# Kernel optimization log

Measured on AMD Instinct MI355X. Metric: run time of the kernel, lower is better.

The kernel has to match this reference:

```python
import jax, jax.numpy as jnp
import numpy as np


def _pairwise_sq_dist(a, b):
    # a: (B,N,D), b: (B,M,D) -> (B,N,M) squared euclidean distances
    # matmul trick matching torch.cdist (clamped at 0 before implicit sqrt)
    a2 = jnp.sum(a * a, axis=-1)  # (B,N)
    b2 = jnp.sum(b * b, axis=-1)  # (B,M)
    ab = jnp.einsum('bnd,bmd->bnm', a, b)  # (B,N,M)
    d2 = a2[:, :, None] + b2[:, None, :] - 2.0 * ab
    return jnp.maximum(d2, 0.0)


def setup_inputs() -> dict:
    key = jax.random.key(0)
    k1, k2 = jax.random.split(key)
    B, N, M, D = 8, 8192, 8192, 3
    gts = jax.random.normal(k1, (B, N, D), dtype=jnp.float32)
    preds = jax.random.normal(k2, (B, M, D), dtype=jnp.float32)
    return {"gts": gts, "preds": preds}


def reference(gts, preds):
    d2 = _pairwise_sq_dist(gts, preds)           # (B,N,M)
    min_g2p = jnp.min(d2, axis=2)                # (B,N) nearest pred for each gt
    min_p2g = jnp.min(d2, axis=1)                # (B,M) nearest gt for each pred
    return jnp.mean(min_g2p) + jnp.mean(min_p2g)
```

## Files before the change

### kernel.cpp

```cpp
#include <hip/hip_runtime.h>
#include <math.h>

#define BB 8
#define NN 8192
#define MM 8192

#define ROWS_PER_BLOCK 256
#define COLS_PER_BLOCK 1024
#define NTILES (COLS_PER_BLOCK / 32)

typedef __attribute__((ext_vector_type(8)))  short short8;
typedef __attribute__((ext_vector_type(16))) float float16;

#define ONE_BF16 ((short)0x3F80)

__device__ inline unsigned short bf16rn(float f) {
    unsigned int u = __float_as_uint(f);
    u += 0x7FFFu + ((u >> 16) & 1u);
    return (unsigned short)(u >> 16);
}
__device__ inline float bf2f(unsigned short h) {
    return __uint_as_float(((unsigned int)h) << 16);
}
__device__ inline float min16(const float16 d) {
    float v = fminf(fminf(d[0], d[1]), d[2]);
    v = fminf(fminf(v, d[3]),  d[4]);
    v = fminf(fminf(v, d[5]),  d[6]);
    v = fminf(fminf(v, d[7]),  d[8]);
    v = fminf(fminf(v, d[9]),  d[10]);
    v = fminf(fminf(v, d[11]), d[12]);
    v = fminf(fminf(v, d[13]), d[14]);
    return fminf(v, d[15]);
}


__global__ __launch_bounds__(512, 4) void chamfer_main(
    const float* __restrict__ gts, const float* __restrict__ preds,
    unsigned int* __restrict__ minn, unsigned int* __restrict__ minp)
{
    __shared__ short8 sBlo[COLS_PER_BLOCK];
    __shared__ short8 sBhi[COLS_PER_BLOCK];
    __shared__ int colmin[COLS_PER_BLOCK];

    const int b       = blockIdx.z;
    const int rowBase = blockIdx.x * ROWS_PER_BLOCK;
    const int colBase = blockIdx.y * COLS_PER_BLOCK;
    const int tid  = threadIdx.x;
    const int lane = tid & 63;
    const int wave = tid >> 6;
    const int h    = lane >> 5;
    const int c    = lane & 31;

    for (int i = tid; i < COLS_PER_BLOCK; i += 512) {
        const float* p = preds + ((size_t)b * MM + colBase + i) * 3;
        float x = p[0], y = p[1], z = p[2];
        float w = x * x + y * y + z * z;
        unsigned short xh = bf16rn(x), yh = bf16rn(y), zh = bf16rn(z);
        unsigned short xl = bf16rn(x - bf2f(xh));
        unsigned short yl = bf16rn(y - bf2f(yh));
        unsigned short zl = bf16rn(z - bf2f(zh));
        unsigned short wh = bf16rn(w);
        unsigned short wl = bf16rn(w - bf2f(wh));
        short8 lo, hi;
        lo[0]=(short)xh; lo[1]=(short)yh; lo[2]=(short)zh; lo[3]=(short)xl;
        lo[4]=(short)yl; lo[5]=(short)zl; lo[6]=(short)xh; lo[7]=(short)yh;
        hi[0]=(short)zh; hi[1]=ONE_BF16;  hi[2]=ONE_BF16;  hi[3]=(short)wh;
        hi[4]=(short)wl; hi[5]=0;         hi[6]=0;         hi[7]=0;
        sBlo[i] = lo; sBhi[i] = hi;
        colmin[i] = 0x7F800000;
    }

    const float* g = gts + ((size_t)b * NN + rowBase + wave * 32 + c) * 3;
    float gx = g[0], gy = g[1], gz = g[2];
    float gw = gx * gx + gy * gy + gz * gz;
    float mx = -2.0f * gx, my = -2.0f * gy, mz = -2.0f * gz;
    unsigned short axh = bf16rn(mx), ayh = bf16rn(my), azh = bf16rn(mz);
    unsigned short axl = bf16rn(mx - bf2f(axh));
    unsigned short ayl = bf16rn(my - bf2f(ayh));
    unsigned short azl = bf16rn(mz - bf2f(azh));
    unsigned short awh = bf16rn(gw);
    unsigned short awl = bf16rn(gw - bf2f(awh));
    short8 alo, ahi;
    alo[0]=(short)axh; alo[1]=(short)ayh; alo[2]=(short)azh; alo[3]=(short)axh;
    alo[4]=(short)ayh; alo[5]=(short)azh; alo[6]=(short)axl; alo[7]=(short)ayl;
    ahi[0]=(short)azl; ahi[1]=(short)awh; ahi[2]=(short)awl; ahi[3]=ONE_BF16;
    ahi[4]=ONE_BF16;   ahi[5]=0;          ahi[6]=0;          ahi[7]=0;
    short8 afrag = h ? ahi : alo;

    float16 zacc;
#pragma unroll
    for (int q = 0; q < 16; ++q) zacc[q] = 0.0f;

    const float kInf = __builtin_inff();
    float rm[16];
#pragma unroll
    for (int q = 0; q < 16; ++q) rm[q] = kInf;

    __syncthreads();

    const short8* myB = h ? sBhi : sBlo;
    for (int t = 0; t < NTILES; t += 2) {
        short8 b0 = myB[t * 32 + c];
        short8 b1 = myB[(t + 1) * 32 + c];
        float16 d0 = __builtin_amdgcn_mfma_f32_32x32x16_bf16(afrag, b0, zacc, 0, 0, 0);
        float16 d1 = __builtin_amdgcn_mfma_f32_32x32x16_bf16(afrag, b1, zacc, 0, 0, 0);
        atomicMin(&colmin[t * 32 + c],       __float_as_int(min16(d0)));
        atomicMin(&colmin[(t + 1) * 32 + c], __float_as_int(min16(d1)));
#pragma unroll
        for (int q = 0; q < 16; ++q)
            rm[q] = fminf(fminf(rm[q], d0[q]), d1[q]);
    }

#pragma unroll
    for (int q = 0; q < 16; ++q) {
        float v = rm[q];
        v = fminf(v, __shfl_xor(v, 1));
        v = fminf(v, __shfl_xor(v, 2));
        v = fminf(v, __shfl_xor(v, 4));
        v = fminf(v, __shfl_xor(v, 8));
        v = fminf(v, __shfl_xor(v, 16));
        rm[q] = v;
    }
    float sel = rm[0];
#pragma unroll
    for (int q = 1; q < 16; ++q) sel = (c == q) ? rm[q] : sel;
    if (c < 16) {
        int rowInTile = (c & 3) + 8 * (c >> 2) + 4 * h;
        unsigned int bits = __float_as_uint(fmaxf(sel, 0.0f));
        atomicMin(&minn[(size_t)b * NN + rowBase + wave * 32 + rowInTile], bits);
    }

    __syncthreads();
    for (int i = tid; i < COLS_PER_BLOCK; i += 512) {
        unsigned int bits = __float_as_uint(fmaxf(__int_as_float(colmin[i]), 0.0f));
        atomicMin(&minp[(size_t)b * MM + colBase + i], bits);
    }
}

__global__ void chamfer_reduce(const unsigned int* __restrict__ minn,
                               const unsigned int* __restrict__ minp,
                               float* __restrict__ accum,
                               unsigned int* __restrict__ ticket,
                               float* __restrict__ out)
{
    const int idx = blockIdx.x * blockDim.x + threadIdx.x;
    const int stride = gridDim.x * blockDim.x;

    float s0 = 0.0f, s1 = 0.0f;
    for (int i = idx; i < BB * NN; i += stride) s0 += __uint_as_float(minn[i]);
    for (int i = idx; i < BB * MM; i += stride) s1 += __uint_as_float(minp[i]);

#pragma unroll
    for (int m = 1; m < 64; m <<= 1) {
        s0 += __shfl_xor(s0, m, 64);
        s1 += __shfl_xor(s1, m, 64);
    }
    __shared__ float w0[4], w1[4];
    if ((threadIdx.x & 63) == 0) {
        w0[threadIdx.x >> 6] = s0;
        w1[threadIdx.x >> 6] = s1;
    }
    __syncthreads();
    if (threadIdx.x == 0) {
        atomicAdd(&accum[0], w0[0] + w0[1] + w0[2] + w0[3]);
        atomicAdd(&accum[1], w1[0] + w1[1] + w1[2] + w1[3]);
        __threadfence();
        unsigned int old = atomicAdd(ticket, 1u);
        unsigned int G = gridDim.x;
        if (old == 0xAAAAAAAAu + G - 1u || old == G - 1u) {
            float a0 = atomicAdd(&accum[0], 0.0f);
            float a1 = atomicAdd(&accum[1], 0.0f);
            out[0] = a0 / (float)(BB * NN) + a1 / (float)(BB * MM);
        }
    }
}

extern "C" void kernel_launch(void* const* d_in, const int* in_sizes, int n_in,
                              void* d_out, int out_size, void* d_ws, size_t ws_size,
                              hipStream_t stream) {
    const float* gts   = (const float*)d_in[0];
    const float* preds = (const float*)d_in[1];
    float* out = (float*)d_out;

    unsigned int* minn   = (unsigned int*)d_ws;
    unsigned int* minp   = minn + (size_t)BB * NN;
    float*        accum  = (float*)(minp + (size_t)BB * MM);
    unsigned int* ticket = (unsigned int*)(accum + 2);

    dim3 grid(NN / ROWS_PER_BLOCK, MM / COLS_PER_BLOCK, BB);
    chamfer_main<<<grid, 512, 0, stream>>>(gts, preds, minn, minp);

    chamfer_reduce<<<64, 256, 0, stream>>>(minn, minp, accum, ticket, out);
}
```

Before: 94.11 us.

## Fuse chamfer into one kernel computing each direction with row-only minima

Replaces the two-kernel design, where one pass did both row minima and LDS atomicMin column minima into global arrays, with a single fused kernel. It launches separate blocks per direction (gts→preds and preds→gts), each scanning all 8192 source points in double-buffered 1024-point LDS chunks. Each block accumulates its row-min sum straight into accum, and a last-block ticket writes the result. This removes LDS atomics, global min arrays and the second reduce launch, at the cost of doing the MFMA distance work twice.

```diff
diff --git a/kernel.cpp b/kernel.cpp
--- a/kernel.cpp
+++ b/kernel.cpp
@@ -1,13 +1,14 @@
 #include <hip/hip_runtime.h>
 #include <math.h>
 
+
 #define BB 8
-#define NN 8192
-#define MM 8192
-
-#define ROWS_PER_BLOCK 256
-#define COLS_PER_BLOCK 1024
-#define NTILES (COLS_PER_BLOCK / 32)
+#define NPTS 8192
+#define ROWS 256
+#define CH 1024
+#define NCHUNK (NPTS / CH)
+#define NTILE (CH / 32)
+#define NBLK ((NPTS / ROWS) * BB * 2)
 
 typedef __attribute__((ext_vector_type(8)))  short short8;
 typedef __attribute__((ext_vector_type(16))) float float16;
@@ -22,55 +23,41 @@
 __device__ inline float bf2f(unsigned short h) {
     return __uint_as_float(((unsigned int)h) << 16);
 }
-__device__ inline float min16(const float16 d) {
-    float v = fminf(fminf(d[0], d[1]), d[2]);
-    v = fminf(fminf(v, d[3]),  d[4]);
-    v = fminf(fminf(v, d[5]),  d[6]);
-    v = fminf(fminf(v, d[7]),  d[8]);
-    v = fminf(fminf(v, d[9]),  d[10]);
-    v = fminf(fminf(v, d[11]), d[12]);
-    v = fminf(fminf(v, d[13]), d[14]);
-    return fminf(v, d[15]);
+
+__device__ inline void packS(float x, float y, float z, short8& lo, short8& hi) {
+    float w = x * x + y * y + z * z;
+    unsigned short xh = bf16rn(x), yh = bf16rn(y), zh = bf16rn(z);
+    unsigned short xl = bf16rn(x - bf2f(xh));
+    unsigned short yl = bf16rn(y - bf2f(yh));
+    unsigned short zl = bf16rn(z - bf2f(zh));
+    unsigned short wh = bf16rn(w), wl = bf16rn(w - bf2f(wh));
+    lo[0]=(short)xh; lo[1]=(short)yh; lo[2]=(short)zh; lo[3]=(short)xl;
+    lo[4]=(short)yl; lo[5]=(short)zl; lo[6]=(short)xh; lo[7]=(short)yh;
+    hi[0]=(short)zh; hi[1]=ONE_BF16;  hi[2]=ONE_BF16;  hi[3]=(short)wh;
+    hi[4]=(short)wl; hi[5]=0;         hi[6]=0;         hi[7]=0;
 }
 
+__global__ __launch_bounds__(512, 4) void chamfer_fused(
+    const float* __restrict__ gts, const float* __restrict__ preds,
+    float* __restrict__ accum, unsigned int* __restrict__ ticket,
+    float* __restrict__ out)
+{
+    __shared__ short8 sB[2][2][CH];
+    __shared__ float wsum[8];
 
-__global__ __launch_bounds__(512, 4) void chamfer_main(
-    const float* __restrict__ gts, const float* __restrict__ preds,
-    unsigned int* __restrict__ minn, unsigned int* __restrict__ minp)
-{
-    __shared__ short8 sBlo[COLS_PER_BLOCK];
-    __shared__ short8 sBhi[COLS_PER_BLOCK];
-    __shared__ int colmin[COLS_PER_BLOCK];
-
-    const int b       = blockIdx.z;
-    const int rowBase = blockIdx.x * ROWS_PER_BLOCK;
-    const int colBase = blockIdx.y * COLS_PER_BLOCK;
+    const int dir     = blockIdx.z;
+    const int b       = blockIdx.y;
+    const int rowBase = blockIdx.x * ROWS;
     const int tid  = threadIdx.x;
     const int lane = tid & 63;
     const int wave = tid >> 6;
     const int h    = lane >> 5;
     const int c    = lane & 31;
 
-    for (int i = tid; i < COLS_PER_BLOCK; i += 512) {
-        const float* p = preds + ((size_t)b * MM + colBase + i) * 3;
-        float x = p[0], y = p[1], z = p[2];
-        float w = x * x + y * y + z * z;
-        unsigned short xh = bf16rn(x), yh = bf16rn(y), zh = bf16rn(z);
-        unsigned short xl = bf16rn(x - bf2f(xh));
-        unsigned short yl = bf16rn(y - bf2f(yh));
-        unsigned short zl = bf16rn(z - bf2f(zh));
-        unsigned short wh = bf16rn(w);
-        unsigned short wl = bf16rn(w - bf2f(wh));
-        short8 lo, hi;
-        lo[0]=(short)xh; lo[1]=(short)yh; lo[2]=(short)zh; lo[3]=(short)xl;
-        lo[4]=(short)yl; lo[5]=(short)zl; lo[6]=(short)xh; lo[7]=(short)yh;
-        hi[0]=(short)zh; hi[1]=ONE_BF16;  hi[2]=ONE_BF16;  hi[3]=(short)wh;
-        hi[4]=(short)wl; hi[5]=0;         hi[6]=0;         hi[7]=0;
-        sBlo[i] = lo; sBhi[i] = hi;
-        colmin[i] = 0x7F800000;
-    }
+    const float* Q  = dir ? preds : gts;
+    const float* Sb = (dir ? gts : preds) + (size_t)b * NPTS * 3;
 
-    const float* g = gts + ((size_t)b * NN + rowBase + wave * 32 + c) * 3;
+    const float* g = Q + ((size_t)b * NPTS + rowBase + wave * 32 + c) * 3;
     float gx = g[0], gy = g[1], gz = g[2];
     float gw = gx * gx + gy * gy + gz * gz;
     float mx = -2.0f * gx, my = -2.0f * gy, mz = -2.0f * gz;
@@ -78,37 +65,61 @@
     unsigned short axl = bf16rn(mx - bf2f(axh));
     unsigned short ayl = bf16rn(my - bf2f(ayh));
     unsigned short azl = bf16rn(mz - bf2f(azh));
-    unsigned short awh = bf16rn(gw);
-    unsigned short awl = bf16rn(gw - bf2f(awh));
+    unsigned short awh = bf16rn(gw), awl = bf16rn(gw - bf2f(awh));
     short8 alo, ahi;
     alo[0]=(short)axh; alo[1]=(short)ayh; alo[2]=(short)azh; alo[3]=(short)axh;
     alo[4]=(short)ayh; alo[5]=(short)azh; alo[6]=(short)axl; alo[7]=(short)ayl;
     ahi[0]=(short)azl; ahi[1]=(short)awh; ahi[2]=(short)awl; ahi[3]=ONE_BF16;
     ahi[4]=ONE_BF16;   ahi[5]=0;          ahi[6]=0;          ahi[7]=0;
-    short8 afrag = h ? ahi : alo;
+    const short8 afrag = h ? ahi : alo;
 
     float16 zacc;
 #pragma unroll
     for (int q = 0; q < 16; ++q) zacc[q] = 0.0f;
 
+    float rm[16];
     const float kInf = __builtin_inff();
-    float rm[16];
 #pragma unroll
     for (int q = 0; q < 16; ++q) rm[q] = kInf;
 
+    float r0x, r0y, r0z, r1x, r1y, r1z;
+    auto loadraw = [&](int ck) {
+        const float* p = Sb + (size_t)(ck * CH + tid) * 3;
+        r0x = p[0]; r0y = p[1]; r0z = p[2];
+        const float* p2 = p + 512 * 3;
+        r1x = p2[0]; r1y = p2[1]; r1z = p2[2];
+    };
+    auto packwrite = [&](int buf) {
+        short8 lo, hi;
+        packS(r0x, r0y, r0z, lo, hi);
+        sB[buf][0][tid] = lo;        sB[buf][1][tid] = hi;
+        packS(r1x, r1y, r1z, lo, hi);
+        sB[buf][0][tid + 512] = lo;  sB[buf][1][tid + 512] = hi;
+    };
+
+    loadraw(0);
+    packwrite(0);
+    loadraw(1);
     __syncthreads();
 
-    const short8* myB = h ? sBhi : sBlo;
-    for (int t = 0; t < NTILES; t += 2) {
-        short8 b0 = myB[t * 32 + c];
-        short8 b1 = myB[(t + 1) * 32 + c];
-        float16 d0 = __builtin_amdgcn_mfma_f32_32x32x16_bf16(afrag, b0, zacc, 0, 0, 0);
-        float16 d1 = __builtin_amdgcn_mfma_f32_32x32x16_bf16(afrag, b1, zacc, 0, 0, 0);
-        atomicMin(&colmin[t * 32 + c],       __float_as_int(min16(d0)));
-        atomicMin(&colmin[(t + 1) * 32 + c], __float_as_int(min16(d1)));
+    for (int ck = 0; ck < NCHUNK; ++ck) {
+        const int buf = ck & 1;
+        if (ck + 1 < NCHUNK) {
+            packwrite(buf ^ 1);
+            if (ck + 2 < NCHUNK) loadraw(ck + 2);
+        }
+        const short8* myB = &sB[buf][h][c];
 #pragma unroll
-        for (int q = 0; q < 16; ++q)
-            rm[q] = fminf(fminf(rm[q], d0[q]), d1[q]);
+        for (int t = 0; t < NTILE; t += 2) {
+            short8 b0 = myB[t * 32];
+            short8 b1 = myB[(t + 1) * 32];
+            float16 d0 = __builtin_amdgcn_mfma_f32_32x32x16_bf16(afrag, b0, zacc, 0, 0, 0);
+            float16 d1 = __builtin_amdgcn_mfma_f32_32x32x16_bf16(afrag, b1, zacc, 0, 0, 0);
+#pragma unroll
+            for (int q = 0; q < 16; ++q)
+                rm[q] = fminf(fminf(rm[q], d0[q]), d1[q]);
+        }
+        __syncthreads();
     }
 
 #pragma unroll
@@ -121,56 +132,24 @@
         v = fminf(v, __shfl_xor(v, 16));
         rm[q] = v;
     }
-    float sel = rm[0];
+    float s = 0.0f;
 #pragma unroll
-    for (int q = 1; q < 16; ++q) sel = (c == q) ? rm[q] : sel;
-    if (c < 16) {
-        int rowInTile = (c & 3) + 8 * (c >> 2) + 4 * h;
-        unsigned int bits = __float_as_uint(fmaxf(sel, 0.0f));
-        atomicMin(&minn[(size_t)b * NN + rowBase + wave * 32 + rowInTile], bits);
-    }
+    for (int q = 0; q < 16; ++q) s += fmaxf(rm[q], 0.0f);
+    s += __shfl_xor(s, 32);
+    if (lane == 0) wsum[wave] = s;
+    __syncthreads();
 
-    __syncthreads();
-    for (int i = tid; i < COLS_PER_BLOCK; i += 512) {
-        unsigned int bits = __float_as_uint(fmaxf(__int_as_float(colmin[i]), 0.0f));
-        atomicMin(&minp[(size_t)b * MM + colBase + i], bits);
-    }
-}
-
-__global__ void chamfer_reduce(const unsigned int* __restrict__ minn,
-                               const unsigned int* __restrict__ minp,
-                               float* __restrict__ accum,
-                               unsigned int* __restrict__ ticket,
-                               float* __restrict__ out)
-{
-    const int idx = blockIdx.x * blockDim.x + threadIdx.x;
-    const int stride = gridDim.x * blockDim.x;
-
-    float s0 = 0.0f, s1 = 0.0f;
-    for (int i = idx; i < BB * NN; i += stride) s0 += __uint_as_float(minn[i]);
-    for (int i = idx; i < BB * MM; i += stride) s1 += __uint_as_float(minp[i]);
-
+    if (tid == 0) {
+        float bs = 0.0f;
 #pragma unroll
-    for (int m = 1; m < 64; m <<= 1) {
-        s0 += __shfl_xor(s0, m, 64);
-        s1 += __shfl_xor(s1, m, 64);
-    }
-    __shared__ float w0[4], w1[4];
-    if ((threadIdx.x & 63) == 0) {
-        w0[threadIdx.x >> 6] = s0;
-        w1[threadIdx.x >> 6] = s1;
-    }
-    __syncthreads();
-    if (threadIdx.x == 0) {
-        atomicAdd(&accum[0], w0[0] + w0[1] + w0[2] + w0[3]);
-        atomicAdd(&accum[1], w1[0] + w1[1] + w1[2] + w1[3]);
+        for (int w = 0; w < 8; ++w) bs += wsum[w];
+        atomicAdd(&accum[dir], bs);
         __threadfence();
         unsigned int old = atomicAdd(ticket, 1u);
-        unsigned int G = gridDim.x;
-        if (old == 0xAAAAAAAAu + G - 1u || old == G - 1u) {
+        if (old == NBLK - 1u || old == 0xAAAAAAAAu + NBLK - 1u) {
             float a0 = atomicAdd(&accum[0], 0.0f);
             float a1 = atomicAdd(&accum[1], 0.0f);
-            out[0] = a0 / (float)(BB * NN) + a1 / (float)(BB * MM);
+            out[0] = (a0 + a1) * (1.0f / (float)(BB * NPTS));
         }
     }
 }
@@ -180,15 +159,10 @@
                               hipStream_t stream) {
     const float* gts   = (const float*)d_in[0];
     const float* preds = (const float*)d_in[1];
-    float* out = (float*)d_out;
 
-    unsigned int* minn   = (unsigned int*)d_ws;
-    unsigned int* minp   = minn + (size_t)BB * NN;
-    float*        accum  = (float*)(minp + (size_t)BB * MM);
+    float*        accum  = (float*)d_ws;
     unsigned int* ticket = (unsigned int*)(accum + 2);
 
-    dim3 grid(NN / ROWS_PER_BLOCK, MM / COLS_PER_BLOCK, BB);
-    chamfer_main<<<grid, 512, 0, stream>>>(gts, preds, minn, minp);
-
-    chamfer_reduce<<<64, 256, 0, stream>>>(minn, minp, accum, ticket, out);
+    dim3 grid(NPTS / ROWS, BB, 2);
+    chamfer_fused<<<grid, 512, 0, stream>>>(gts, preds, accum, ticket, (float*)d_out);
 }
```

Measured after the change: 95.83 us. About the same (+1.8%).

## Give each wave two row tiles and merge column minima into global atomics

Applied to the files above, without the earlier changes.

Each wave now handles 64 gt rows as two A fragments and reuses each loaded B fragment for both, which halves the LDS reads per MFMA. The shared-memory column-min buffer and its LDS atomics are removed. Column minima are combined across the two row tiles and both half-waves with a shuffle, then written straight to global memory with atomicMin for each tile pair. Row reductions switch from shfl_xor to DPP row ops and min3-style trees. The trade-off is many more global atomics and higher register pressure from the doubled running-min arrays.

```diff
diff --git a/kernel.cpp b/kernel.cpp
--- a/kernel.cpp
+++ b/kernel.cpp
@@ -1,13 +1,12 @@
 #include <hip/hip_runtime.h>
 #include <math.h>
 
+
 #define BB 8
-#define NN 8192
-#define MM 8192
-
-#define ROWS_PER_BLOCK 256
-#define COLS_PER_BLOCK 1024
-#define NTILES (COLS_PER_BLOCK / 32)
+#define NPTS 8192
+#define ROWS 512
+#define CH 1024
+#define NPAIR (CH / 64)
 
 typedef __attribute__((ext_vector_type(8)))  short short8;
 typedef __attribute__((ext_vector_type(16))) float float16;
@@ -22,118 +21,141 @@
 __device__ inline float bf2f(unsigned short h) {
     return __uint_as_float(((unsigned int)h) << 16);
 }
+__device__ inline float min3f(float a, float b, float c) {
+    return fminf(fminf(a, b), c);
+}
 __device__ inline float min16(const float16 d) {
-    float v = fminf(fminf(d[0], d[1]), d[2]);
-    v = fminf(fminf(v, d[3]),  d[4]);
-    v = fminf(fminf(v, d[5]),  d[6]);
-    v = fminf(fminf(v, d[7]),  d[8]);
-    v = fminf(fminf(v, d[9]),  d[10]);
-    v = fminf(fminf(v, d[11]), d[12]);
-    v = fminf(fminf(v, d[13]), d[14]);
-    return fminf(v, d[15]);
-}
-
+    float t0 = min3f(d[0],  d[1],  d[2]);
+    float t1 = min3f(d[3],  d[4],  d[5]);
+    float t2 = min3f(d[6],  d[7],  d[8]);
+    float t3 = min3f(d[9],  d[10], d[11]);
+    float t4 = min3f(d[12], d[13], d[14]);
+    return fminf(min3f(t0, t1, t2), min3f(t3, t4, d[15]));
+}
+
+#define DPP_FMIN(v, CTRL) do {                                                \
+    int _s = __builtin_amdgcn_update_dpp(__float_as_int(v), __float_as_int(v),\
+                                         (CTRL), 0xf, 0xf, false);            \
+    (v) = fminf((v), __int_as_float(_s)); } while (0)
+
+__device__ inline void packB(float x, float y, float z, short8& lo, short8& hi) {
+    float w = x * x + y * y + z * z;
+    unsigned short xh = bf16rn(x), yh = bf16rn(y), zh = bf16rn(z);
+    unsigned short xl = bf16rn(x - bf2f(xh));
+    unsigned short yl = bf16rn(y - bf2f(yh));
+    unsigned short zl = bf16rn(z - bf2f(zh));
+    unsigned short wh = bf16rn(w), wl = bf16rn(w - bf2f(wh));
+    lo[0]=(short)xh; lo[1]=(short)yh; lo[2]=(short)zh; lo[3]=(short)xl;
+    lo[4]=(short)yl; lo[5]=(short)zl; lo[6]=(short)xh; lo[7]=(short)yh;
+    hi[0]=(short)zh; hi[1]=ONE_BF16;  hi[2]=ONE_BF16;  hi[3]=(short)wh;
+    hi[4]=(short)wl; hi[5]=0;         hi[6]=0;         hi[7]=0;
+}
+__device__ inline void packA(float x, float y, float z, short8& lo, short8& hi) {
+    float w = x * x + y * y + z * z;
+    float mx = -2.0f * x, my = -2.0f * y, mz = -2.0f * z;
+    unsigned short xh = bf16rn(mx), yh = bf16rn(my), zh = bf16rn(mz);
+    unsigned short xl = bf16rn(mx - bf2f(xh));
+    unsigned short yl = bf16rn(my - bf2f(yh));
+    unsigned short zl = bf16rn(mz - bf2f(zh));
+    unsigned short wh = bf16rn(w), wl = bf16rn(w - bf2f(wh));
+    lo[0]=(short)xh; lo[1]=(short)yh; lo[2]=(short)zh; lo[3]=(short)xh;
+    lo[4]=(short)yh; lo[5]=(short)zh; lo[6]=(short)xl; lo[7]=(short)yl;
+    hi[0]=(short)zl; hi[1]=(short)wh; hi[2]=(short)wl; hi[3]=ONE_BF16;
+    hi[4]=ONE_BF16;  hi[5]=0;         hi[6]=0;         hi[7]=0;
+}
 
 __global__ __launch_bounds__(512, 4) void chamfer_main(
     const float* __restrict__ gts, const float* __restrict__ preds,
     unsigned int* __restrict__ minn, unsigned int* __restrict__ minp)
 {
-    __shared__ short8 sBlo[COLS_PER_BLOCK];
-    __shared__ short8 sBhi[COLS_PER_BLOCK];
-    __shared__ int colmin[COLS_PER_BLOCK];
+    __shared__ short8 sB[2][CH];
 
     const int b       = blockIdx.z;
-    const int rowBase = blockIdx.x * ROWS_PER_BLOCK;
-    const int colBase = blockIdx.y * COLS_PER_BLOCK;
+    const int rowBase = blockIdx.x * ROWS;
+    const int colBase = blockIdx.y * CH;
     const int tid  = threadIdx.x;
     const int lane = tid & 63;
     const int wave = tid >> 6;
     const int h    = lane >> 5;
     const int c    = lane & 31;
 
-    for (int i = tid; i < COLS_PER_BLOCK; i += 512) {
-        const float* p = preds + ((size_t)b * MM + colBase + i) * 3;
-        float x = p[0], y = p[1], z = p[2];
-        float w = x * x + y * y + z * z;
-        unsigned short xh = bf16rn(x), yh = bf16rn(y), zh = bf16rn(z);
-        unsigned short xl = bf16rn(x - bf2f(xh));
-        unsigned short yl = bf16rn(y - bf2f(yh));
-        unsigned short zl = bf16rn(z - bf2f(zh));
-        unsigned short wh = bf16rn(w);
-        unsigned short wl = bf16rn(w - bf2f(wh));
+    for (int i = tid; i < CH; i += 512) {
+        const float* p = preds + ((size_t)b * NPTS + colBase + i) * 3;
         short8 lo, hi;
-        lo[0]=(short)xh; lo[1]=(short)yh; lo[2]=(short)zh; lo[3]=(short)xl;
-        lo[4]=(short)yl; lo[5]=(short)zl; lo[6]=(short)xh; lo[7]=(short)yh;
-        hi[0]=(short)zh; hi[1]=ONE_BF16;  hi[2]=ONE_BF16;  hi[3]=(short)wh;
-        hi[4]=(short)wl; hi[5]=0;         hi[6]=0;         hi[7]=0;
-        sBlo[i] = lo; sBhi[i] = hi;
-        colmin[i] = 0x7F800000;
-    }
-
-    const float* g = gts + ((size_t)b * NN + rowBase + wave * 32 + c) * 3;
-    float gx = g[0], gy = g[1], gz = g[2];
-    float gw = gx * gx + gy * gy + gz * gz;
-    float mx = -2.0f * gx, my = -2.0f * gy, mz = -2.0f * gz;
-    unsigned short axh = bf16rn(mx), ayh = bf16rn(my), azh = bf16rn(mz);
-    unsigned short axl = bf16rn(mx - bf2f(axh));
-    unsigned short ayl = bf16rn(my - bf2f(ayh));
-    unsigned short azl = bf16rn(mz - bf2f(azh));
-    unsigned short awh = bf16rn(gw);
-    unsigned short awl = bf16rn(gw - bf2f(awh));
-    short8 alo, ahi;
-    alo[0]=(short)axh; alo[1]=(short)ayh; alo[2]=(short)azh; alo[3]=(short)axh;
-    alo[4]=(short)ayh; alo[5]=(short)azh; alo[6]=(short)axl; alo[7]=(short)ayl;
-    ahi[0]=(short)azl; ahi[1]=(short)awh; ahi[2]=(short)awl; ahi[3]=ONE_BF16;
-    ahi[4]=ONE_BF16;   ahi[5]=0;          ahi[6]=0;          ahi[7]=0;
-    short8 afrag = h ? ahi : alo;
+        packB(p[0], p[1], p[2], lo, hi);
+        sB[0][i] = lo; sB[1][i] = hi;
+    }
+
+    short8 a[2];
+    {
+        const float* g = gts + ((size_t)b * NPTS + rowBase + wave * 64 + c) * 3;
+#pragma unroll
+        for (int r = 0; r < 2; ++r) {
+            short8 lo, hi;
+            packA(g[r*96], g[r*96+1], g[r*96+2], lo, hi);
+            a[r] = h ? hi : lo;
+        }
+    }
 
     float16 zacc;
 #pragma unroll
     for (int q = 0; q < 16; ++q) zacc[q] = 0.0f;
 
     const float kInf = __builtin_inff();
-    float rm[16];
-#pragma unroll
-    for (int q = 0; q < 16; ++q) rm[q] = kInf;
+    float rm[2][16];
+#pragma unroll
+    for (int r = 0; r < 2; ++r)
+#pragma unroll
+        for (int q = 0; q < 16; ++q) rm[r][q] = kInf;
 
     __syncthreads();
 
-    const short8* myB = h ? sBhi : sBlo;
-    for (int t = 0; t < NTILES; t += 2) {
-        short8 b0 = myB[t * 32 + c];
-        short8 b1 = myB[(t + 1) * 32 + c];
-        float16 d0 = __builtin_amdgcn_mfma_f32_32x32x16_bf16(afrag, b0, zacc, 0, 0, 0);
-        float16 d1 = __builtin_amdgcn_mfma_f32_32x32x16_bf16(afrag, b1, zacc, 0, 0, 0);
-        atomicMin(&colmin[t * 32 + c],       __float_as_int(min16(d0)));
-        atomicMin(&colmin[(t + 1) * 32 + c], __float_as_int(min16(d1)));
-#pragma unroll
-        for (int q = 0; q < 16; ++q)
-            rm[q] = fminf(fminf(rm[q], d0[q]), d1[q]);
-    }
-
-#pragma unroll
-    for (int q = 0; q < 16; ++q) {
-        float v = rm[q];
-        v = fminf(v, __shfl_xor(v, 1));
-        v = fminf(v, __shfl_xor(v, 2));
-        v = fminf(v, __shfl_xor(v, 4));
-        v = fminf(v, __shfl_xor(v, 8));
-        v = fminf(v, __shfl_xor(v, 16));
-        rm[q] = v;
-    }
-    float sel = rm[0];
-#pragma unroll
-    for (int q = 1; q < 16; ++q) sel = (c == q) ? rm[q] : sel;
-    if (c < 16) {
-        int rowInTile = (c & 3) + 8 * (c >> 2) + 4 * h;
-        unsigned int bits = __float_as_uint(fmaxf(sel, 0.0f));
-        atomicMin(&minn[(size_t)b * NN + rowBase + wave * 32 + rowInTile], bits);
-    }
-
-    __syncthreads();
-    for (int i = tid; i < COLS_PER_BLOCK; i += 512) {
-        unsigned int bits = __float_as_uint(fmaxf(__int_as_float(colmin[i]), 0.0f));
-        atomicMin(&minp[(size_t)b * MM + colBase + i], bits);
+    unsigned int* minp_b = minp + (size_t)b * NPTS + colBase;
+    const short8* myB = &sB[h][c];
+
+#pragma unroll 2
+    for (int tp = 0; tp < NPAIR; ++tp) {
+        short8 b0 = myB[tp * 64];
+        short8 b1 = myB[tp * 64 + 32];
+        float16 d0 = __builtin_amdgcn_mfma_f32_32x32x16_bf16(a[0], b0, zacc, 0, 0, 0);
+        float16 d1 = __builtin_amdgcn_mfma_f32_32x32x16_bf16(a[0], b1, zacc, 0, 0, 0);
+#pragma unroll
+        for (int q = 0; q < 16; ++q) rm[0][q] = min3f(rm[0][q], d0[q], d1[q]);
+        float c0 = min16(d0);
+        float c1 = min16(d1);
+        d0 = __builtin_amdgcn_mfma_f32_32x32x16_bf16(a[1], b0, zacc, 0, 0, 0);
+        d1 = __builtin_amdgcn_mfma_f32_32x32x16_bf16(a[1], b1, zacc, 0, 0, 0);
+#pragma unroll
+        for (int q = 0; q < 16; ++q) rm[1][q] = min3f(rm[1][q], d0[q], d1[q]);
+        c0 = fminf(c0, min16(d0));
+        c1 = fminf(c1, min16(d1));
+        c0 = fminf(c0, __shfl_xor(c0, 32));
+        c1 = fminf(c1, __shfl_xor(c1, 32));
+        float cv = h ? c1 : c0;
+        atomicMin(&minp_b[tp * 64 + lane], __float_as_uint(fmaxf(cv, 0.0f)));
+    }
+
+#pragma unroll
+    for (int r = 0; r < 2; ++r)
+#pragma unroll
+        for (int q = 0; q < 16; ++q) {
+            float v = rm[r][q];
+            DPP_FMIN(v, 0x111);
+            DPP_FMIN(v, 0x112);
+            DPP_FMIN(v, 0x114);
+            DPP_FMIN(v, 0x118);
+            DPP_FMIN(v, 0x142);
+            rm[r][q] = v;
+        }
+    if ((lane & 31) == 31) {
+        unsigned int* mb = minn + (size_t)b * NPTS + rowBase + wave * 64;
+#pragma unroll
+        for (int r = 0; r < 2; ++r)
+#pragma unroll
+            for (int q = 0; q < 16; ++q) {
+                int row = r * 32 + (q & 3) + 8 * (q >> 2) + 4 * h;
+                atomicMin(&mb[row], __float_as_uint(fmaxf(rm[r][q], 0.0f)));
+            }
     }
 }
 
@@ -147,8 +169,8 @@
     const int stride = gridDim.x * blockDim.x;
 
     float s0 = 0.0f, s1 = 0.0f;
-    for (int i = idx; i < BB * NN; i += stride) s0 += __uint_as_float(minn[i]);
-    for (int i = idx; i < BB * MM; i += stride) s1 += __uint_as_float(minp[i]);
+    for (int i = idx; i < BB * NPTS; i += stride) s0 += __uint_as_float(minn[i]);
+    for (int i = idx; i < BB * NPTS; i += stride) s1 += __uint_as_float(minp[i]);
 
 #pragma unroll
     for (int m = 1; m < 64; m <<= 1) {
@@ -170,7 +192,7 @@
         if (old == 0xAAAAAAAAu + G - 1u || old == G - 1u) {
             float a0 = atomicAdd(&accum[0], 0.0f);
             float a1 = atomicAdd(&accum[1], 0.0f);
-            out[0] = a0 / (float)(BB * NN) + a1 / (float)(BB * MM);
+            out[0] = a0 / (float)(BB * NPTS) + a1 / (float)(BB * NPTS);
         }
     }
 }
@@ -183,11 +205,11 @@
     float* out = (float*)d_out;
 
     unsigned int* minn   = (unsigned int*)d_ws;
-    unsigned int* minp   = minn + (size_t)BB * NN;
-    float*        accum  = (float*)(minp + (size_t)BB * MM);
+    unsigned int* minp   = minn + (size_t)BB * NPTS;
+    float*        accum  = (float*)(minp + (size_t)BB * NPTS);
     unsigned int* ticket = (unsigned int*)(accum + 2);
 
-    dim3 grid(NN / ROWS_PER_BLOCK, MM / COLS_PER_BLOCK, BB);
+    dim3 grid(NPTS / ROWS, NPTS / CH, BB);
     chamfer_main<<<grid, 512, 0, stream>>>(gts, preds, minn, minp);
 
     chamfer_reduce<<<64, 256, 0, stream>>>(minn, minp, accum, ticket, out);
```

Result: slower. 105.1 us (+11.7%).
